# Kernel tuning notes

Measured on AMD Instinct MI355X. Metric: run time of the kernel, lower is better.

Reference implementation:

```python
import jax, jax.numpy as jnp
import numpy as np

B, T, C, H = 8, 2048, 1024, 64


def build_rope_cache(seq_len, dim):
    half = dim // 2
    inv_freq = 1.0 / (10000.0 ** (jnp.arange(half, dtype=jnp.float32) / half))
    t = jnp.arange(seq_len, dtype=jnp.float32)
    freqs = t[:, None] * inv_freq[None, :]          # (T, half)
    cos = jnp.repeat(jnp.cos(freqs), 2, axis=-1)    # (T, dim) interleaved
    sin = jnp.repeat(jnp.sin(freqs), 2, axis=-1)
    return cos, sin


def apply_rope(x, cos, sin):
    # x: (B, T, H); cos/sin: (T, H)
    x1 = x[..., ::2]
    x2 = x[..., 1::2]
    rot = jnp.stack([-x2, x1], axis=-1).reshape(x.shape)
    return x * cos[None] + rot * sin[None]


def setup_inputs() -> dict:
    key = jax.random.key(0)
    kx, kq, kk, kv = jax.random.split(key, 4)
    scale = 1.0 / np.sqrt(C)
    return {
        "x": jax.random.normal(kx, (B, T, C), dtype=jnp.float32),
        "Wq": jax.random.normal(kq, (C, H), dtype=jnp.float32) * scale,
        "Wk": jax.random.normal(kk, (C, H), dtype=jnp.float32) * scale,
        "Wv": jax.random.normal(kv, (C, H), dtype=jnp.float32) * scale,
    }


def reference(x, Wq, Wk, Wv):
    Bc, Tc, _ = x.shape
    head_size = Wq.shape[1]
    cos, sin = build_rope_cache(Tc, head_size)

    q = apply_rope(x @ Wq, cos, sin)   # (B, T, H)
    k = apply_rope(x @ Wk, cos, sin)   # (B, T, H)
    v = x @ Wv                          # (B, T, H)

    # full TxT masked softmax attention (matches original non-fused path)
    wei = jnp.einsum('bth,bsh->bts', q, k) * (head_size ** -0.5)  # (B, T, T)
    causal = jnp.tril(jnp.ones((Tc, Tc), dtype=bool))
    wei = jnp.where(causal[None], wei, -jnp.inf)
    wei = jax.nn.softmax(wei, axis=-1)
    # dropout p=0 (eval mode) -> identity
    return jnp.einsum('bts,bsh->bth', wei, v)
```

## Files before the change

kernel.cpp:

```cpp
#include <hip/hip_runtime.h>
#include <cmath>

#define Tn  2048
#define Cn  1024
#define Hn  64
#define BTn 16384

typedef _Float16 f16x8 __attribute__((ext_vector_type(8)));
typedef _Float16 f16x4 __attribute__((ext_vector_type(4)));
typedef _Float16 f16x2 __attribute__((ext_vector_type(2)));
typedef float    f32x4 __attribute__((ext_vector_type(4)));

__global__ __launch_bounds__(256) void prep_w_kernel(
    const float* __restrict__ Wq, const float* __restrict__ Wk,
    const float* __restrict__ Wv, _Float16* __restrict__ Wt)
{
    __shared__ float ts[64][65];
    const int blk = blockIdx.x;
    const int p   = blk >> 4;
    const int c0  = (blk & 15) * 64;
    const float* __restrict__ W = (p == 0) ? Wq : (p == 1) ? Wk : Wv;
    const int tid = threadIdx.x;
    #pragma unroll
    for (int it = 0; it < 16; it++) {
        int idx = tid + it * 256;
        int c = idx >> 6, n = idx & 63;
        ts[c][n] = W[(size_t)(c0 + c) * Hn + n];
    }
    __syncthreads();
    #pragma unroll
    for (int it = 0; it < 16; it++) {
        int idx = tid + it * 256;
        int n = idx >> 6, c = idx & 63;
        Wt[(size_t)(p * 64 + n) * Cn + c0 + c] = (_Float16)ts[c][n];
    }
}

#define XSP 1032

__global__ __launch_bounds__(512, 4) void proj_kernel(
    const float* __restrict__ x, const _Float16* __restrict__ Wt,
    _Float16* __restrict__ qh, _Float16* __restrict__ kh_out, _Float16* __restrict__ vT)
{
    __shared__ __align__(16) _Float16 xs[32 * XSP];
    const int row0 = blockIdx.x * 32;
    const int tid  = threadIdx.x;
    const int wave = tid >> 6, lane = tid & 63;
    const int kh   = wave >> 2;
    const int wc   = wave & 3;
    const int quad = lane >> 4, l15 = lane & 15;

    #pragma unroll 8
    for (int it = 0; it < 16; it++) {
        int idx = tid + it * 512;
        int r = idx >> 8, c4 = idx & 255;
        float4 xv = *(const float4*)&x[(size_t)(row0 + r) * Cn + c4 * 4];
        f16x4 hv = { (_Float16)xv.x, (_Float16)xv.y, (_Float16)xv.z, (_Float16)xv.w };
        *(f16x4*)&xs[r * XSP + c4 * 4] = hv;
    }
    __syncthreads();

    f32x4 acc[2][3] = {};
    const _Float16* __restrict__ wb = Wt + (size_t)(wc * 48 + l15) * Cn
                                         + kh * 512 + quad * 8;
    const _Float16* __restrict__ xp = &xs[kh * 512 + quad * 8];

    #pragma unroll 4
    for (int kc = 0; kc < 512; kc += 32) {
        f16x8 b0 = *(const f16x8*)&wb[kc];
        f16x8 b1 = *(const f16x8*)&wb[16 * Cn + kc];
        f16x8 b2 = *(const f16x8*)&wb[32 * Cn + kc];
        f16x8 a0 = *(const f16x8*)&xp[(     l15) * XSP + kc];
        f16x8 a1 = *(const f16x8*)&xp[(16 + l15) * XSP + kc];
        acc[0][0] = __builtin_amdgcn_mfma_f32_16x16x32_f16(a0, b0, acc[0][0], 0, 0, 0);
        acc[1][0] = __builtin_amdgcn_mfma_f32_16x16x32_f16(a1, b0, acc[1][0], 0, 0, 0);
        acc[0][1] = __builtin_amdgcn_mfma_f32_16x16x32_f16(a0, b1, acc[0][1], 0, 0, 0);
        acc[1][1] = __builtin_amdgcn_mfma_f32_16x16x32_f16(a1, b1, acc[1][1], 0, 0, 0);
        acc[0][2] = __builtin_amdgcn_mfma_f32_16x16x32_f16(a0, b2, acc[0][2], 0, 0, 0);
        acc[1][2] = __builtin_amdgcn_mfma_f32_16x16x32_f16(a1, b2, acc[1][2], 0, 0, 0);
    }

    __syncthreads();
    f32x4* __restrict__ pbuf = (f32x4*)xs;
    if (kh) {
        #pragma unroll
        for (int mt = 0; mt < 2; mt++)
            #pragma unroll
            for (int nt = 0; nt < 3; nt++)
                pbuf[(mt * 3 + nt) * 256 + wc * 64 + lane] = acc[mt][nt];
    }
    __syncthreads();
    if (kh) return;
    #pragma unroll
    for (int mt = 0; mt < 2; mt++)
        #pragma unroll
        for (int nt = 0; nt < 3; nt++)
            acc[mt][nt] += pbuf[(mt * 3 + nt) * 256 + wc * 64 + lane];

    const int bidx = row0 >> 11;
    #pragma unroll
    for (int nt = 0; nt < 3; nt++) {
        const int n = wc * 48 + nt * 16 + l15;
        const int p = n >> 6;
        const int h = n & 63;
        if (p < 2) {
            _Float16* __restrict__ outb = (p == 0) ? qh : kh_out;
            const float invf = __expf(-0.2878231366242557f * (float)(h >> 1));
            #pragma unroll
            for (int mt = 0; mt < 2; mt++) {
                #pragma unroll
                for (int r = 0; r < 4; r++) {
                    int   row = row0 + mt * 16 + quad * 4 + r;
                    float val = acc[mt][nt][r];
                    float partner = __shfl_xor(val, 1, 64);
                    float ang = (float)(row & (Tn - 1)) * invf;
                    float sv, cv;
                    __sincosf(ang, &sv, &cv);
                    float res = (h & 1) ? fmaf(val, cv,  partner * sv)
                                        : fmaf(val, cv, -partner * sv);
                    if (p == 0) res *= 0.125f;
                    float resn = __shfl_xor(res, 1, 64);
                    if (!(l15 & 1)) {
                        f16x2 pk = { (_Float16)res, (_Float16)resn };
                        *(f16x2*)&outb[(size_t)row * Hn + h] = pk;
                    }
                }
            }
        } else {
            #pragma unroll
            for (int mt = 0; mt < 2; mt++) {
                int t = (row0 & (Tn - 1)) + mt * 16 + quad * 4;
                f16x4 pv = { (_Float16)acc[mt][nt][0], (_Float16)acc[mt][nt][1],
                             (_Float16)acc[mt][nt][2], (_Float16)acc[mt][nt][3] };
                *(f16x4*)&vT[((size_t)bidx * Hn + h) * Tn + t] = pv;
            }
        }
    }
}

#define PSP 72

__global__ __launch_bounds__(256, 4) void attn_kernel(
    const _Float16* __restrict__ qh, const _Float16* __restrict__ kh,
    const _Float16* __restrict__ vT, float* __restrict__ out)
{
    __shared__ _Float16 ps[4][16 * PSP];
    __shared__ float ocomb[4][16][65];
    __shared__ float mlcomb[4][2][16];

    const int blk = blockIdx.x;
    const int b   = blk & 7;
    const int j   = blk >> 3;
    const int jm  = j & 31, g = j >> 5;
    const int qt  = (g == 0) ? (127 - jm)
                  : (g == 1) ? (64 + jm)
                  : (g == 2) ? (63 - jm) : jm;
    const int t0  = qt * 16;
    const int tid = threadIdx.x;
    const int w = tid >> 6, lane = tid & 63;
    const int quad = lane >> 4, l15 = lane & 15;

    const _Float16* __restrict__ qb = qh + (size_t)b * Tn * Hn;
    const _Float16* __restrict__ kb = kh + (size_t)b * Tn * Hn;
    const _Float16* __restrict__ vb = vT + (size_t)b * Hn * Tn;

    const f16x8 aq0 = *(const f16x8*)&qb[(size_t)(t0 + l15) * Hn +      quad * 8];
    const f16x8 aq1 = *(const f16x8*)&qb[(size_t)(t0 + l15) * Hn + 32 + quad * 8];

    float m_run[4], l_run[4];
    f32x4 oacc[4] = {};
    #pragma unroll
    for (int r = 0; r < 4; r++) { m_run[r] = -1e30f; l_run[r] = 0.0f; }

    const int nst = (t0 + 16 + 63) >> 6;
    for (int jt = w; jt < nst; jt += 4) {
        const int s0 = jt * 64;

        f16x8 kf[4][2];
        #pragma unroll
        for (int nt = 0; nt < 4; nt++) {
            const _Float16* kp = &kb[(size_t)(s0 + nt * 16 + l15) * Hn + quad * 8];
            kf[nt][0] = *(const f16x8*)kp;
            kf[nt][1] = *(const f16x8*)(kp + 32);
        }
        f32x4 sacc[4];
        #pragma unroll
        for (int nt = 0; nt < 4; nt++) {
            f32x4 z = {};
            z = __builtin_amdgcn_mfma_f32_16x16x32_f16(aq0, kf[nt][0], z, 0, 0, 0);
            z = __builtin_amdgcn_mfma_f32_16x16x32_f16(aq1, kf[nt][1], z, 0, 0, 0);
            sacc[nt] = z;
        }

        f16x8 vf[2][4];
        #pragma unroll
        for (int sc = 0; sc < 2; sc++)
            #pragma unroll
            for (int ht = 0; ht < 4; ht++)
                vf[sc][ht] = *(const f16x8*)&vb[(size_t)(ht * 16 + l15) * Tn
                                                + s0 + sc * 32 + quad * 8];

        if (jt == nst - 1) {
            #pragma unroll
            for (int nt = 0; nt < 4; nt++)
                #pragma unroll
                for (int r = 0; r < 4; r++) {
                    int scol = s0 + nt * 16 + l15;
                    int trow = t0 + quad * 4 + r;
                    if (scol > trow) sacc[nt][r] = -1e30f;
                }
        }

        float pr[4][4];
        #pragma unroll
        for (int r = 0; r < 4; r++) {
            float mx = fmaxf(fmaxf(sacc[0][r], sacc[1][r]),
                             fmaxf(sacc[2][r], sacc[3][r]));
            #pragma unroll
            for (int off = 1; off < 16; off <<= 1)
                mx = fmaxf(mx, __shfl_xor(mx, off, 64));
            float mnew  = fmaxf(m_run[r], mx);
            float alpha = __expf(m_run[r] - mnew);
            m_run[r] = mnew;
            float rs = 0.0f;
            #pragma unroll
            for (int nt = 0; nt < 4; nt++) {
                float pv = __expf(sacc[nt][r] - mnew);
                pr[nt][r] = pv; rs += pv;
            }
            #pragma unroll
            for (int off = 1; off < 16; off <<= 1)
                rs += __shfl_xor(rs, off, 64);
            l_run[r] = fmaf(l_run[r], alpha, rs);
            #pragma unroll
            for (int ht = 0; ht < 4; ht++)
                oacc[ht][r] = oacc[ht][r] * alpha;
        }

        #pragma unroll
        for (int nt = 0; nt < 4; nt++)
            #pragma unroll
            for (int r = 0; r < 4; r++) {
                float pv = pr[nt][r];
                float pn = __shfl_xor(pv, 1, 64);
                if (!(l15 & 1)) {
                    f16x2 pk = { (_Float16)pv, (_Float16)pn };
                    *(f16x2*)&ps[w][(quad * 4 + r) * PSP + nt * 16 + l15] = pk;
                }
            }

        #pragma unroll
        for (int sc = 0; sc < 2; sc++) {
            f16x8 ap = *(const f16x8*)&ps[w][l15 * PSP + sc * 32 + quad * 8];
            #pragma unroll
            for (int ht = 0; ht < 4; ht++)
                oacc[ht] = __builtin_amdgcn_mfma_f32_16x16x32_f16(ap, vf[sc][ht],
                                                                  oacc[ht], 0, 0, 0);
        }
    }

    #pragma unroll
    for (int r = 0; r < 4; r++) {
        #pragma unroll
        for (int ht = 0; ht < 4; ht++)
            ocomb[w][quad * 4 + r][ht * 16 + l15] = oacc[ht][r];
        if (l15 == 0) {
            mlcomb[w][0][quad * 4 + r] = m_run[r];
            mlcomb[w][1][quad * 4 + r] = l_run[r];
        }
    }
    __syncthreads();

    #pragma unroll
    for (int rp = 0; rp < 4; rp++) {
        int row = w * 4 + rp;
        float m0 = mlcomb[0][0][row], m1 = mlcomb[1][0][row];
        float m2 = mlcomb[2][0][row], m3 = mlcomb[3][0][row];
        float mm = fmaxf(fmaxf(m0, m1), fmaxf(m2, m3));
        float a0 = __expf(m0 - mm), a1 = __expf(m1 - mm);
        float a2 = __expf(m2 - mm), a3 = __expf(m3 - mm);
        float ll = mlcomb[0][1][row] * a0 + mlcomb[1][1][row] * a1
                 + mlcomb[2][1][row] * a2 + mlcomb[3][1][row] * a3;
        float ov = (ocomb[0][row][lane] * a0 + ocomb[1][row][lane] * a1
                  + ocomb[2][row][lane] * a2 + ocomb[3][row][lane] * a3) / ll;
        out[((size_t)b * Tn + t0 + row) * Hn + lane] = ov;
    }
}

extern "C" void kernel_launch(void* const* d_in, const int* in_sizes, int n_in,
                              void* d_out, int out_size, void* d_ws, size_t ws_size,
                              hipStream_t stream) {
    const float* x  = (const float*)d_in[0];
    const float* Wq = (const float*)d_in[1];
    const float* Wk = (const float*)d_in[2];
    const float* Wv = (const float*)d_in[3];

    const size_t qkvN = (size_t)BTn * Hn;
    _Float16* qh = (_Float16*)d_ws;
    _Float16* kh = qh + qkvN;
    _Float16* vT = kh + qkvN;
    _Float16* Wt = vT + qkvN;

    prep_w_kernel<<<48, 256, 0, stream>>>(Wq, Wk, Wv, Wt);
    proj_kernel<<<BTn / 32, 512, 0, stream>>>(x, Wt, qh, kh, vT);
    attn_kernel<<<1024, 256, 0, stream>>>(qh, kh, vT, (float*)d_out);
}
```

Baseline: 155.6 us.

## Software-pipeline loads in projection and attention kernels with register prefetch

```diff
diff --git a/kernel.cpp b/kernel.cpp
--- a/kernel.cpp
+++ b/kernel.cpp
@@ -10,6 +10,8 @@
 typedef _Float16 f16x4 __attribute__((ext_vector_type(4)));
 typedef _Float16 f16x2 __attribute__((ext_vector_type(2)));
 typedef float    f32x4 __attribute__((ext_vector_type(4)));
+
+#define MFMA16(a, b, c) __builtin_amdgcn_mfma_f32_16x16x32_f16(a, b, c, 0, 0, 0)
 
 __global__ __launch_bounds__(256) void prep_w_kernel(
     const float* __restrict__ Wq, const float* __restrict__ Wk,
@@ -50,13 +52,22 @@
     const int wc   = wave & 3;
     const int quad = lane >> 4, l15 = lane & 15;
 
-    #pragma unroll 8
-    for (int it = 0; it < 16; it++) {
-        int idx = tid + it * 512;
-        int r = idx >> 8, c4 = idx & 255;
-        float4 xv = *(const float4*)&x[(size_t)(row0 + r) * Cn + c4 * 4];
-        f16x4 hv = { (_Float16)xv.x, (_Float16)xv.y, (_Float16)xv.z, (_Float16)xv.w };
-        *(f16x4*)&xs[r * XSP + c4 * 4] = hv;
+    {
+        float4 xv[16];
+        #pragma unroll
+        for (int it = 0; it < 16; it++) {
+            int idx = tid + it * 512;
+            int r = idx >> 8, c4 = idx & 255;
+            xv[it] = *(const float4*)&x[(size_t)(row0 + r) * Cn + c4 * 4];
+        }
+        #pragma unroll
+        for (int it = 0; it < 16; it++) {
+            int idx = tid + it * 512;
+            int r = idx >> 8, c4 = idx & 255;
+            f16x4 hv = { (_Float16)xv[it].x, (_Float16)xv[it].y,
+                         (_Float16)xv[it].z, (_Float16)xv[it].w };
+            *(f16x4*)&xs[r * XSP + c4 * 4] = hv;
+        }
     }
     __syncthreads();
 
@@ -65,19 +76,32 @@
                                          + kh * 512 + quad * 8;
     const _Float16* __restrict__ xp = &xs[kh * 512 + quad * 8];
 
-    #pragma unroll 4
-    for (int kc = 0; kc < 512; kc += 32) {
-        f16x8 b0 = *(const f16x8*)&wb[kc];
-        f16x8 b1 = *(const f16x8*)&wb[16 * Cn + kc];
-        f16x8 b2 = *(const f16x8*)&wb[32 * Cn + kc];
-        f16x8 a0 = *(const f16x8*)&xp[(     l15) * XSP + kc];
-        f16x8 a1 = *(const f16x8*)&xp[(16 + l15) * XSP + kc];
-        acc[0][0] = __builtin_amdgcn_mfma_f32_16x16x32_f16(a0, b0, acc[0][0], 0, 0, 0);
-        acc[1][0] = __builtin_amdgcn_mfma_f32_16x16x32_f16(a1, b0, acc[1][0], 0, 0, 0);
-        acc[0][1] = __builtin_amdgcn_mfma_f32_16x16x32_f16(a0, b1, acc[0][1], 0, 0, 0);
-        acc[1][1] = __builtin_amdgcn_mfma_f32_16x16x32_f16(a1, b1, acc[1][1], 0, 0, 0);
-        acc[0][2] = __builtin_amdgcn_mfma_f32_16x16x32_f16(a0, b2, acc[0][2], 0, 0, 0);
-        acc[1][2] = __builtin_amdgcn_mfma_f32_16x16x32_f16(a1, b2, acc[1][2], 0, 0, 0);
+    f16x8 bb[3][3], ab[3][2];
+    #pragma unroll
+    for (int p = 0; p < 3; p++) {
+        bb[p][0] = *(const f16x8*)&wb[p * 32];
+        bb[p][1] = *(const f16x8*)&wb[16 * Cn + p * 32];
+        bb[p][2] = *(const f16x8*)&wb[32 * Cn + p * 32];
+        ab[p][0] = *(const f16x8*)&xp[(     l15) * XSP + p * 32];
+        ab[p][1] = *(const f16x8*)&xp[(16 + l15) * XSP + p * 32];
+    }
+    #pragma unroll
+    for (int kc = 0; kc < 16; kc++) {
+        const int s = kc % 3;
+        acc[0][0] = MFMA16(ab[s][0], bb[s][0], acc[0][0]);
+        acc[1][0] = MFMA16(ab[s][1], bb[s][0], acc[1][0]);
+        acc[0][1] = MFMA16(ab[s][0], bb[s][1], acc[0][1]);
+        acc[1][1] = MFMA16(ab[s][1], bb[s][1], acc[1][1]);
+        acc[0][2] = MFMA16(ab[s][0], bb[s][2], acc[0][2]);
+        acc[1][2] = MFMA16(ab[s][1], bb[s][2], acc[1][2]);
+        if (kc + 3 < 16) {
+            const int kn = (kc + 3) * 32;
+            bb[s][0] = *(const f16x8*)&wb[kn];
+            bb[s][1] = *(const f16x8*)&wb[16 * Cn + kn];
+            bb[s][2] = *(const f16x8*)&wb[32 * Cn + kn];
+            ab[s][0] = *(const f16x8*)&xp[(     l15) * XSP + kn];
+            ab[s][1] = *(const f16x8*)&xp[(16 + l15) * XSP + kn];
+        }
     }
 
     __syncthreads();
@@ -173,24 +197,20 @@
     for (int r = 0; r < 4; r++) { m_run[r] = -1e30f; l_run[r] = 0.0f; }
 
     const int nst = (t0 + 16 + 63) >> 6;
+
+    f16x8 kfA[4][2];
+    if (w < nst) {
+        const int s0 = w * 64;
+        #pragma unroll
+        for (int nt = 0; nt < 4; nt++) {
+            const _Float16* kp = &kb[(size_t)(s0 + nt * 16 + l15) * Hn + quad * 8];
+            kfA[nt][0] = *(const f16x8*)kp;
+            kfA[nt][1] = *(const f16x8*)(kp + 32);
+        }
+    }
+
     for (int jt = w; jt < nst; jt += 4) {
         const int s0 = jt * 64;
-
-        f16x8 kf[4][2];
-        #pragma unroll
-        for (int nt = 0; nt < 4; nt++) {
-            const _Float16* kp = &kb[(size_t)(s0 + nt * 16 + l15) * Hn + quad * 8];
-            kf[nt][0] = *(const f16x8*)kp;
-            kf[nt][1] = *(const f16x8*)(kp + 32);
-        }
-        f32x4 sacc[4];
-        #pragma unroll
-        for (int nt = 0; nt < 4; nt++) {
-            f32x4 z = {};
-            z = __builtin_amdgcn_mfma_f32_16x16x32_f16(aq0, kf[nt][0], z, 0, 0, 0);
-            z = __builtin_amdgcn_mfma_f32_16x16x32_f16(aq1, kf[nt][1], z, 0, 0, 0);
-            sacc[nt] = z;
-        }
 
         f16x8 vf[2][4];
         #pragma unroll
@@ -199,6 +219,26 @@
             for (int ht = 0; ht < 4; ht++)
                 vf[sc][ht] = *(const f16x8*)&vb[(size_t)(ht * 16 + l15) * Tn
                                                 + s0 + sc * 32 + quad * 8];
+
+        f16x8 kfB[4][2];
+        {
+            const int sp = (jt + 4 < nst) ? (jt + 4) * 64 : s0;
+            #pragma unroll
+            for (int nt = 0; nt < 4; nt++) {
+                const _Float16* kp = &kb[(size_t)(sp + nt * 16 + l15) * Hn + quad * 8];
+                kfB[nt][0] = *(const f16x8*)kp;
+                kfB[nt][1] = *(const f16x8*)(kp + 32);
+            }
+        }
+
+        f32x4 sacc[4];
+        #pragma unroll
+        for (int nt = 0; nt < 4; nt++) {
+            f32x4 z = {};
+            z = MFMA16(aq0, kfA[nt][0], z);
+            z = MFMA16(aq1, kfA[nt][1], z);
+            sacc[nt] = z;
+        }
 
         if (jt == nst - 1) {
             #pragma unroll
@@ -254,8 +294,13 @@
             f16x8 ap = *(const f16x8*)&ps[w][l15 * PSP + sc * 32 + quad * 8];
             #pragma unroll
             for (int ht = 0; ht < 4; ht++)
-                oacc[ht] = __builtin_amdgcn_mfma_f32_16x16x32_f16(ap, vf[sc][ht],
-                                                                  oacc[ht], 0, 0, 0);
+                oacc[ht] = MFMA16(ap, vf[sc][ht], oacc[ht]);
+        }
+
+        #pragma unroll
+        for (int nt = 0; nt < 4; nt++) {
+            kfA[nt][0] = kfB[nt][0];
+            kfA[nt][1] = kfB[nt][1];
         }
     }
 
```

Result: slower. 176.9 us (+13.7%).

## Stage x tiles via direct global-to-LDS loads with XOR swizzle in projection

Applied to the files above, without the earlier changes.

```diff
diff --git a/kernel.cpp b/kernel.cpp
--- a/kernel.cpp
+++ b/kernel.cpp
@@ -10,6 +10,14 @@
 typedef _Float16 f16x4 __attribute__((ext_vector_type(4)));
 typedef _Float16 f16x2 __attribute__((ext_vector_type(2)));
 typedef float    f32x4 __attribute__((ext_vector_type(4)));
+
+#define MFMA16(a, b, c) __builtin_amdgcn_mfma_f32_16x16x32_f16(a, b, c, 0, 0, 0)
+
+__device__ __forceinline__ void gload16(const void* g, void* l) {
+    __builtin_amdgcn_global_load_lds(
+        (const __attribute__((address_space(1))) void*)g,
+        (__attribute__((address_space(3))) void*)l, 16, 0, 0);
+}
 
 __global__ __launch_bounds__(256) void prep_w_kernel(
     const float* __restrict__ Wq, const float* __restrict__ Wk,
@@ -36,13 +44,24 @@
     }
 }
 
-#define XSP 1032
+__device__ __forceinline__ f16x8 ldsA(const char* xb, int row, int col) {
+    int lb = row * 2048 + col * 4;
+    int sw = (row & 7) << 4;
+    f32x4 lo = *(const f32x4*)(xb + ((lb     ) ^ sw));
+    f32x4 hi = *(const f32x4*)(xb + ((lb + 16) ^ sw));
+    f16x8 r;
+    r[0] = (_Float16)lo[0]; r[1] = (_Float16)lo[1];
+    r[2] = (_Float16)lo[2]; r[3] = (_Float16)lo[3];
+    r[4] = (_Float16)hi[0]; r[5] = (_Float16)hi[1];
+    r[6] = (_Float16)hi[2]; r[7] = (_Float16)hi[3];
+    return r;
+}
 
 __global__ __launch_bounds__(512, 4) void proj_kernel(
     const float* __restrict__ x, const _Float16* __restrict__ Wt,
     _Float16* __restrict__ qh, _Float16* __restrict__ kh_out, _Float16* __restrict__ vT)
 {
-    __shared__ __align__(16) _Float16 xs[32 * XSP];
+    __shared__ __align__(16) float xsf[32 * 512];
     const int row0 = blockIdx.x * 32;
     const int tid  = threadIdx.x;
     const int wave = tid >> 6, lane = tid & 63;
@@ -50,38 +69,46 @@
     const int wc   = wave & 3;
     const int quad = lane >> 4, l15 = lane & 15;
 
-    #pragma unroll 8
-    for (int it = 0; it < 16; it++) {
-        int idx = tid + it * 512;
-        int r = idx >> 8, c4 = idx & 255;
-        float4 xv = *(const float4*)&x[(size_t)(row0 + r) * Cn + c4 * 4];
-        f16x4 hv = { (_Float16)xv.x, (_Float16)xv.y, (_Float16)xv.z, (_Float16)xv.w };
-        *(f16x4*)&xs[r * XSP + c4 * 4] = hv;
-    }
+    f32x4 acc[2][3] = {};
+    const _Float16* __restrict__ wb = Wt + (size_t)(wc * 48 + l15) * Cn + quad * 8;
+    const char* xb = (const char*)xsf;
+
+    #pragma unroll
+    for (int ph = 0; ph < 2; ph++) {
+        if (ph) __syncthreads();
+
+        {
+            const char* xg = (const char*)x + ((size_t)row0 * Cn + ph * 512) * 4;
+            char* lb0 = (char*)xsf + wave * 1024;
+            #pragma unroll
+            for (int r2 = 0; r2 < 8; r2++) {
+                int lbl  = tid * 16 + r2 * 8192;
+                int row  = lbl >> 11;
+                int colb = (lbl & 2047) ^ ((row & 7) << 4);
+                gload16(xg + (size_t)row * (Cn * 4) + colb, lb0 + r2 * 8192);
+            }
+        }
+        __syncthreads();
+
+        #pragma unroll
+        for (int kc = 0; kc < 8; kc++) {
+            const int kf = kh * 256 + kc * 32;
+            f16x8 b0 = *(const f16x8*)&wb[ph * 512 + kf];
+            f16x8 b1 = *(const f16x8*)&wb[16 * Cn + ph * 512 + kf];
+            f16x8 b2 = *(const f16x8*)&wb[32 * Cn + ph * 512 + kf];
+            f16x8 a0 = ldsA(xb,      l15, kf + quad * 8);
+            f16x8 a1 = ldsA(xb, 16 + l15, kf + quad * 8);
+            acc[0][0] = MFMA16(a0, b0, acc[0][0]);
+            acc[1][0] = MFMA16(a1, b0, acc[1][0]);
+            acc[0][1] = MFMA16(a0, b1, acc[0][1]);
+            acc[1][1] = MFMA16(a1, b1, acc[1][1]);
+            acc[0][2] = MFMA16(a0, b2, acc[0][2]);
+            acc[1][2] = MFMA16(a1, b2, acc[1][2]);
+        }
+    }
+
     __syncthreads();
-
-    f32x4 acc[2][3] = {};
-    const _Float16* __restrict__ wb = Wt + (size_t)(wc * 48 + l15) * Cn
-                                         + kh * 512 + quad * 8;
-    const _Float16* __restrict__ xp = &xs[kh * 512 + quad * 8];
-
-    #pragma unroll 4
-    for (int kc = 0; kc < 512; kc += 32) {
-        f16x8 b0 = *(const f16x8*)&wb[kc];
-        f16x8 b1 = *(const f16x8*)&wb[16 * Cn + kc];
-        f16x8 b2 = *(const f16x8*)&wb[32 * Cn + kc];
-        f16x8 a0 = *(const f16x8*)&xp[(     l15) * XSP + kc];
-        f16x8 a1 = *(const f16x8*)&xp[(16 + l15) * XSP + kc];
-        acc[0][0] = __builtin_amdgcn_mfma_f32_16x16x32_f16(a0, b0, acc[0][0], 0, 0, 0);
-        acc[1][0] = __builtin_amdgcn_mfma_f32_16x16x32_f16(a1, b0, acc[1][0], 0, 0, 0);
-        acc[0][1] = __builtin_amdgcn_mfma_f32_16x16x32_f16(a0, b1, acc[0][1], 0, 0, 0);
-        acc[1][1] = __builtin_amdgcn_mfma_f32_16x16x32_f16(a1, b1, acc[1][1], 0, 0, 0);
-        acc[0][2] = __builtin_amdgcn_mfma_f32_16x16x32_f16(a0, b2, acc[0][2], 0, 0, 0);
-        acc[1][2] = __builtin_amdgcn_mfma_f32_16x16x32_f16(a1, b2, acc[1][2], 0, 0, 0);
-    }
-
-    __syncthreads();
-    f32x4* __restrict__ pbuf = (f32x4*)xs;
+    f32x4* __restrict__ pbuf = (f32x4*)xsf;
     if (kh) {
         #pragma unroll
         for (int mt = 0; mt < 2; mt++)
@@ -187,8 +214,8 @@
         #pragma unroll
         for (int nt = 0; nt < 4; nt++) {
             f32x4 z = {};
-            z = __builtin_amdgcn_mfma_f32_16x16x32_f16(aq0, kf[nt][0], z, 0, 0, 0);
-            z = __builtin_amdgcn_mfma_f32_16x16x32_f16(aq1, kf[nt][1], z, 0, 0, 0);
+            z = MFMA16(aq0, kf[nt][0], z);
+            z = MFMA16(aq1, kf[nt][1], z);
             sacc[nt] = z;
         }
 
@@ -254,8 +281,7 @@
             f16x8 ap = *(const f16x8*)&ps[w][l15 * PSP + sc * 32 + quad * 8];
             #pragma unroll
             for (int ht = 0; ht < 4; ht++)
-                oacc[ht] = __builtin_amdgcn_mfma_f32_16x16x32_f16(ap, vf[sc][ht],
-                                                                  oacc[ht], 0, 0, 0);
+                oacc[ht] = MFMA16(ap, vf[sc][ht], oacc[ht]);
         }
     }
 
```

Measured after the change: 156.5 us. Within noise of the previous version (+0.5%).

## Software-pipeline weight loads in projection GEMM with inline-asm global loads

Applied to the files above, without the earlier changes.

```diff
diff --git a/kernel.cpp b/kernel.cpp
--- a/kernel.cpp
+++ b/kernel.cpp
@@ -10,6 +10,8 @@
 typedef _Float16 f16x4 __attribute__((ext_vector_type(4)));
 typedef _Float16 f16x2 __attribute__((ext_vector_type(2)));
 typedef float    f32x4 __attribute__((ext_vector_type(4)));
+
+#define MFMA16(a, b, c) __builtin_amdgcn_mfma_f32_16x16x32_f16(a, b, c, 0, 0, 0)
 
 __global__ __launch_bounds__(256) void prep_w_kernel(
     const float* __restrict__ Wq, const float* __restrict__ Wk,
@@ -38,7 +40,7 @@
 
 #define XSP 1032
 
-__global__ __launch_bounds__(512, 4) void proj_kernel(
+__global__ __launch_bounds__(512) void proj_kernel(
     const float* __restrict__ x, const _Float16* __restrict__ Wt,
     _Float16* __restrict__ qh, _Float16* __restrict__ kh_out, _Float16* __restrict__ vT)
 {
@@ -50,35 +52,78 @@
     const int wc   = wave & 3;
     const int quad = lane >> 4, l15 = lane & 15;
 
-    #pragma unroll 8
-    for (int it = 0; it < 16; it++) {
-        int idx = tid + it * 512;
-        int r = idx >> 8, c4 = idx & 255;
-        float4 xv = *(const float4*)&x[(size_t)(row0 + r) * Cn + c4 * 4];
-        f16x4 hv = { (_Float16)xv.x, (_Float16)xv.y, (_Float16)xv.z, (_Float16)xv.w };
-        *(f16x4*)&xs[r * XSP + c4 * 4] = hv;
+    {
+        f32x4 xv[16];
+        #pragma unroll
+        for (int it = 0; it < 16; it++) {
+            int idx = tid + it * 512;
+            int r = idx >> 8, c4 = idx & 255;
+            const float* ap = &x[(size_t)(row0 + r) * Cn + c4 * 4];
+            asm volatile("global_load_dwordx4 %0, %1, off"
+                         : "=v"(xv[it]) : "v"(ap));
+        }
+        asm volatile("s_waitcnt vmcnt(0)" ::: "memory");
+        __builtin_amdgcn_sched_barrier(0);
+        #pragma unroll
+        for (int it = 0; it < 16; it++) {
+            int idx = tid + it * 512;
+            int r = idx >> 8, c4 = idx & 255;
+            f16x4 hv = { (_Float16)xv[it][0], (_Float16)xv[it][1],
+                         (_Float16)xv[it][2], (_Float16)xv[it][3] };
+            *(f16x4*)&xs[r * XSP + c4 * 4] = hv;
+        }
     }
     __syncthreads();
 
     f32x4 acc[2][3] = {};
-    const _Float16* __restrict__ wb = Wt + (size_t)(wc * 48 + l15) * Cn
-                                         + kh * 512 + quad * 8;
-    const _Float16* __restrict__ xp = &xs[kh * 512 + quad * 8];
-
-    #pragma unroll 4
-    for (int kc = 0; kc < 512; kc += 32) {
-        f16x8 b0 = *(const f16x8*)&wb[kc];
-        f16x8 b1 = *(const f16x8*)&wb[16 * Cn + kc];
-        f16x8 b2 = *(const f16x8*)&wb[32 * Cn + kc];
-        f16x8 a0 = *(const f16x8*)&xp[(     l15) * XSP + kc];
-        f16x8 a1 = *(const f16x8*)&xp[(16 + l15) * XSP + kc];
-        acc[0][0] = __builtin_amdgcn_mfma_f32_16x16x32_f16(a0, b0, acc[0][0], 0, 0, 0);
-        acc[1][0] = __builtin_amdgcn_mfma_f32_16x16x32_f16(a1, b0, acc[1][0], 0, 0, 0);
-        acc[0][1] = __builtin_amdgcn_mfma_f32_16x16x32_f16(a0, b1, acc[0][1], 0, 0, 0);
-        acc[1][1] = __builtin_amdgcn_mfma_f32_16x16x32_f16(a1, b1, acc[1][1], 0, 0, 0);
-        acc[0][2] = __builtin_amdgcn_mfma_f32_16x16x32_f16(a0, b2, acc[0][2], 0, 0, 0);
-        acc[1][2] = __builtin_amdgcn_mfma_f32_16x16x32_f16(a1, b2, acc[1][2], 0, 0, 0);
-    }
+    const _Float16* __restrict__ wb0 = Wt + (size_t)(wc * 48 + l15) * Cn
+                                          + kh * 512 + quad * 8;
+    const _Float16* __restrict__ wb1 = wb0 + 16 * Cn;
+    const _Float16* __restrict__ wb2 = wb0 + 32 * Cn;
+    const _Float16* __restrict__ xp  = &xs[kh * 512 + quad * 8];
+
+    f16x8 bb[4][3];
+
+    #define ISSUE_STEP(kcn)  {                                                 \
+        asm volatile("global_load_dwordx4 %0, %1, off"                         \
+                     : "=v"(bb[(kcn) & 3][0]) : "v"(wb0 + (kcn) * 32));        \
+        asm volatile("global_load_dwordx4 %0, %1, off"                         \
+                     : "=v"(bb[(kcn) & 3][1]) : "v"(wb1 + (kcn) * 32));        \
+        asm volatile("global_load_dwordx4 %0, %1, off"                         \
+                     : "=v"(bb[(kcn) & 3][2]) : "v"(wb2 + (kcn) * 32)); }
+
+    #define COMPUTE_STEP(kcn, NWAIT)  {                                        \
+        f16x8 a0 = *(const f16x8*)&xp[(     l15) * XSP + (kcn) * 32];          \
+        f16x8 a1 = *(const f16x8*)&xp[(16 + l15) * XSP + (kcn) * 32];          \
+        asm volatile("s_waitcnt vmcnt(" #NWAIT ")" ::: "memory");              \
+        __builtin_amdgcn_sched_barrier(0);                                     \
+        acc[0][0] = MFMA16(a0, bb[(kcn) & 3][0], acc[0][0]);                   \
+        acc[1][0] = MFMA16(a1, bb[(kcn) & 3][0], acc[1][0]);                   \
+        acc[0][1] = MFMA16(a0, bb[(kcn) & 3][1], acc[0][1]);                   \
+        acc[1][1] = MFMA16(a1, bb[(kcn) & 3][1], acc[1][1]);                   \
+        acc[0][2] = MFMA16(a0, bb[(kcn) & 3][2], acc[0][2]);                   \
+        acc[1][2] = MFMA16(a1, bb[(kcn) & 3][2], acc[1][2]); }
+
+    ISSUE_STEP(0)  ISSUE_STEP(1)  ISSUE_STEP(2)
+    ISSUE_STEP(3)  COMPUTE_STEP(0, 9)
+    ISSUE_STEP(4)  COMPUTE_STEP(1, 9)
+    ISSUE_STEP(5)  COMPUTE_STEP(2, 9)
+    ISSUE_STEP(6)  COMPUTE_STEP(3, 9)
+    ISSUE_STEP(7)  COMPUTE_STEP(4, 9)
+    ISSUE_STEP(8)  COMPUTE_STEP(5, 9)
+    ISSUE_STEP(9)  COMPUTE_STEP(6, 9)
+    ISSUE_STEP(10) COMPUTE_STEP(7, 9)
+    ISSUE_STEP(11) COMPUTE_STEP(8, 9)
+    ISSUE_STEP(12) COMPUTE_STEP(9, 9)
+    ISSUE_STEP(13) COMPUTE_STEP(10, 9)
+    ISSUE_STEP(14) COMPUTE_STEP(11, 9)
+    ISSUE_STEP(15) COMPUTE_STEP(12, 9)
+    COMPUTE_STEP(13, 6)
+    COMPUTE_STEP(14, 3)
+    COMPUTE_STEP(15, 0)
+
+    #undef ISSUE_STEP
+    #undef COMPUTE_STEP
 
     __syncthreads();
     f32x4* __restrict__ pbuf = (f32x4*)xs;
@@ -187,8 +232,8 @@
         #pragma unroll
         for (int nt = 0; nt < 4; nt++) {
             f32x4 z = {};
-            z = __builtin_amdgcn_mfma_f32_16x16x32_f16(aq0, kf[nt][0], z, 0, 0, 0);
-            z = __builtin_amdgcn_mfma_f32_16x16x32_f16(aq1, kf[nt][1], z, 0, 0, 0);
+            z = MFMA16(aq0, kf[nt][0], z);
+            z = MFMA16(aq1, kf[nt][1], z);
             sacc[nt] = z;
         }
 
@@ -254,8 +299,7 @@
             f16x8 ap = *(const f16x8*)&ps[w][l15 * PSP + sc * 32 + quad * 8];
             #pragma unroll
             for (int ht = 0; ht < 4; ht++)
-                oacc[ht] = __builtin_amdgcn_mfma_f32_16x16x32_f16(ap, vf[sc][ht],
-                                                                  oacc[ht], 0, 0, 0);
+                oacc[ht] = MFMA16(ap, vf[sc][ht], oacc[ht]);
         }
     }
 
```

Result: no change. 155.9 us (+0.2%).
